# Optimization experiments

Hardware: AMD Instinct MI355X
Metric: run time of the kernel (lower is better)

The kernel has to match this reference:

```python
import jax, jax.numpy as jnp
import numpy as np

V, E_DIM, H_DIR, D_A, C = 50000, 300, 512, 512, 8921  # vocab, embed dim, LSTM hidden per dir, attn dim, classes
B, S = 8, 2048
RNN = 2 * H_DIR  # bidirectional output dim = rnn_dim = 1024


def setup_inputs() -> dict:
    key = jax.random.key(0)
    ks = jax.random.split(key, 13)
    sc = lambda k, shape, s=0.05: (jax.random.normal(k, shape, jnp.float32) * s)
    return {
        "text": jax.random.randint(ks[0], (B, S), 0, V),
        "length": jnp.full((B,), S, dtype=jnp.int32),  # full-length seqs: packing is identity
        "embed": sc(ks[1], (V, E_DIM), 0.1),
        # PyTorch LSTM params, gate order (i, f, g, o); bias folded: b = b_ih + b_hh
        "Wih_f": sc(ks[2], (4 * H_DIR, E_DIM)),
        "Whh_f": sc(ks[3], (4 * H_DIR, H_DIR)),
        "b_f": sc(ks[4], (4 * H_DIR,)),
        "Wih_b": sc(ks[5], (4 * H_DIR, E_DIM)),
        "Whh_b": sc(ks[6], (4 * H_DIR, H_DIR)),
        "b_b": sc(ks[7], (4 * H_DIR,)),
        "Ww": sc(ks[8], (D_A, RNN)),   # self.W: Linear(rnn_dim, d_a, bias=False)
        "Qw": sc(ks[9], (C, D_A)),     # self.Q: Linear(d_a, num_classes, bias=False)
        "Ow": sc(ks[10], (C, RNN)),    # self.output.weight
        "Ob": sc(ks[11], (C,)),        # self.output.bias
    }


def _lstm(x_sbe, Wih, Whh, b, reverse):
    # x_sbe: [S, B, E]; returns hidden states [S, B, H]
    xw = jnp.einsum('sbe,ge->sbg', x_sbe, Wih) + b  # precompute input projections [S,B,4H]
    H = Whh.shape[1]
    Bsz = x_sbe.shape[1]

    def step(carry, g_in):
        h, c = carry
        g = g_in + h @ Whh.T
        i, f, gg, o = jnp.split(g, 4, axis=-1)
        c = jax.nn.sigmoid(f) * c + jax.nn.sigmoid(i) * jnp.tanh(gg)
        h = jax.nn.sigmoid(o) * jnp.tanh(c)
        return (h, c), h

    init = (jnp.zeros((Bsz, H), x_sbe.dtype), jnp.zeros((Bsz, H), x_sbe.dtype))
    _, hs = jax.lax.scan(step, init, xw, reverse=reverse)
    return hs


def reference(text, length, embed, Wih_f, Whh_f, b_f, Wih_b, Whh_b, b_b, Ww, Qw, Ow, Ob):
    # Embedding (eval mode: dropout is identity)
    x = embed[text]                                   # [B,S,E]
    xs = jnp.swapaxes(x, 0, 1)                        # [S,B,E]
    hf = _lstm(xs, Wih_f, Whh_f, b_f, reverse=False)  # [S,B,H]
    hb = _lstm(xs, Wih_b, Whh_b, b_b, reverse=True)   # [S,B,H]
    H = jnp.swapaxes(jnp.concatenate([hf, hb], axis=-1), 0, 1)  # [B,S,rnn_dim]
    # Label-wise attention
    Z = jnp.tanh(jnp.einsum('bsd,ad->bsa', H, Ww))    # [B,S,d_a]
    scores = jnp.einsum('ca,bsa->bcs', Qw, Z)         # [B,C,S]
    alpha = jax.nn.softmax(scores, axis=2)            # softmax over seq
    E = jnp.einsum('bcs,bsd->bcd', alpha, H)          # [B,C,rnn_dim]
    logits = jnp.einsum('cd,bcd->bc', Ow, E) + Ob     # [B,C]
    return logits, alpha
```

## Files before the change

kernel.cpp:

```cpp
#include <hip/hip_runtime.h>
#include <hip/hip_bf16.h>

typedef __attribute__((ext_vector_type(4))) float f32x4;
typedef __attribute__((ext_vector_type(8))) short s16x8;
typedef __attribute__((ext_vector_type(4))) short s16x4;

#define DI __device__ __forceinline__

static constexpr int B_ = 8, S_ = 2048, E_ = 300, EP_ = 320, HD_ = 512, G4_ = 2048;
static constexpr int C_ = 8921, RNN_ = 1024, NROW_ = 16384;

DI float bf2f(unsigned short u){ unsigned int x = ((unsigned int)u) << 16; return __builtin_bit_cast(float, x); }
DI unsigned short f2bf(float f){
  unsigned int x = __builtin_bit_cast(unsigned int, f);
  x += 0x7fff + ((x >> 16) & 1);
  return (unsigned short)(x >> 16);
}
DI float sigm(float x){ return 1.f / (1.f + __expf(-x)); }
DI float tanh_f(float x){
  x = fminf(fmaxf(x, -15.f), 15.f);
  float e = __expf(2.f * x);
  return (e - 1.f) / (e + 1.f);
}
DI void gload16(const void* g, void* l){
  __builtin_amdgcn_global_load_lds((const __attribute__((address_space(1))) void*)g,
                                   (__attribute__((address_space(3))) void*)l, 16, 0, 0);
}
DI unsigned has_sent(unsigned x){
  return (unsigned)(((x & 0xFFFFu) == 0xFFFFu) | ((x >> 16) == 0xFFFFu));
}

__global__ void k_cvt_pad(const float* __restrict__ src, unsigned short* __restrict__ dst,
                          int Rs, int Cs, int Cd){
  int r = blockIdx.x;
  long db = (long)r * Cd;
  for (int c = threadIdx.x; c < Cd; c += blockDim.x){
    float v = (r < Rs && c < Cs) ? src[(long)r * Cs + c] : 0.f;
    dst[db + c] = f2bf(v);
  }
}

__global__ void k_embed(const int* __restrict__ text, const float* __restrict__ emb,
                        unsigned short* __restrict__ xe){
  int m = blockIdx.x;
  int s = m >> 3, b = m & 7;
  int tok = text[b * S_ + s];
  const float* e = emb + (long)tok * E_;
  long db = (long)m * EP_;
  for (int c = threadIdx.x; c < EP_; c += blockDim.x){
    float v = (c < E_) ? e[c] : 0.f;
    xe[db + c] = f2bf(v);
  }
}

template<int EPI>
__global__ __launch_bounds__(256, 2)
void k_gemm_bt(const unsigned short* __restrict__ A, const unsigned short* __restrict__ Bt,
               void* __restrict__ Cout, int N, int K, int Mreal,
               long aBatch, long bBatch, long cBatch, const float* __restrict__ bias){
  __shared__ unsigned short As[128 * 32];
  __shared__ unsigned short Bs[128 * 32];
  const int tid = threadIdx.x, lane = tid & 63, wid = tid >> 6;
  const int wm = wid >> 1, wn = wid & 1;
  const int bm0 = blockIdx.y * 128, bn0 = blockIdx.x * 128;
  A  += (long)blockIdx.z * aBatch;
  Bt += (long)blockIdx.z * bBatch;

  f32x4 acc[4][4];
#pragma unroll
  for (int i = 0; i < 4; ++i)
#pragma unroll
    for (int jx = 0; jx < 4; ++jx) acc[i][jx] = f32x4{0.f, 0.f, 0.f, 0.f};

  for (int k0 = 0; k0 < K; k0 += 32){
    __syncthreads();
#pragma unroll
    for (int cc = 0; cc < 2; ++cc){
      int e = tid + cc * 256;
      int row = e >> 2, seg = e & 3;
      const unsigned short* ga = A + ((long)(bm0 + row)) * K + k0 + seg * 8;
      gload16(ga, (char*)As + cc * 4096 + wid * 1024);
      const unsigned short* gb = Bt + ((long)(bn0 + row)) * K + k0 + seg * 8;
      gload16(gb, (char*)Bs + cc * 4096 + wid * 1024);
    }
    __syncthreads();
    s16x8 af[4], bfr[4];
#pragma unroll
    for (int mt = 0; mt < 4; ++mt){
      int arow = wm * 64 + mt * 16 + (lane & 15);
      af[mt] = *(const s16x8*)((const char*)As + arow * 64 + (lane >> 4) * 16);
    }
#pragma unroll
    for (int nt = 0; nt < 4; ++nt){
      int brow = wn * 64 + nt * 16 + (lane & 15);
      bfr[nt] = *(const s16x8*)((const char*)Bs + brow * 64 + (lane >> 4) * 16);
    }
#pragma unroll
    for (int mt = 0; mt < 4; ++mt)
#pragma unroll
      for (int nt = 0; nt < 4; ++nt)
        acc[mt][nt] = __builtin_amdgcn_mfma_f32_16x16x32_bf16(af[mt], bfr[nt], acc[mt][nt], 0, 0, 0);
  }

  long co = (long)blockIdx.z * cBatch;
#pragma unroll
  for (int mt = 0; mt < 4; ++mt){
#pragma unroll
    for (int r = 0; r < 4; ++r){
      int row = bm0 + wm * 64 + mt * 16 + (lane >> 4) * 4 + r;
      if (row < Mreal){
#pragma unroll
        for (int nt = 0; nt < 4; ++nt){
          int col = bn0 + wn * 64 + nt * 16 + (lane & 15);
          float v = acc[mt][nt][r];
          long idx = co + (long)row * N + col;
          if constexpr (EPI == 0) ((float*)Cout)[idx] = v;
          else if constexpr (EPI == 1) ((unsigned short*)Cout)[idx] = f2bf(tanh_f(v));
          else if constexpr (EPI == 2) ((unsigned short*)Cout)[idx] = f2bf(v + bias[col]);
          else ((unsigned short*)Cout)[idx] = f2bf(v);
        }
      }
    }
  }
}

__global__ __launch_bounds__(256, 1)
void k_lstm(const unsigned short* __restrict__ xw_all,
            const float* __restrict__ Whh_f, const float* __restrict__ Whh_b,
            unsigned short* __restrict__ Hb){
  __shared__ unsigned short hA[16 * 512];
  __shared__ float gl[8 * 128];
  char* hAc = (char*)hA;
  const int tid = threadIdx.x, lane = tid & 63, wave = tid >> 6;
  const int wg = blockIdx.x;
  const int dir = wg >> 4, w16 = wg & 15;
  const int j0 = w16 * 32;
  const int b8 = tid >> 5, j = tid & 31;
  const float* Whh = dir ? Whh_b : Whh_f;
  const unsigned short* xw = xw_all + (long)dir * NROW_ * G4_;

  s16x8 Bf0[16], Bf1[16];
  {
    int lr0 = wave * 32 + (lane & 15);
    int lr1 = lr0 + 16;
    int kg = (lane >> 4) * 8;
    const float* r0 = Whh + (long)((lr0 >> 5) * 512 + j0 + (lr0 & 31)) * 512;
    const float* r1 = Whh + (long)((lr1 >> 5) * 512 + j0 + (lr1 & 31)) * 512;
#pragma unroll
    for (int kt = 0; kt < 16; ++kt){
      s16x8 v0, v1;
#pragma unroll
      for (int i = 0; i < 8; ++i){
        v0[i] = (short)f2bf(r0[kt * 32 + kg + i]);
        v1[i] = (short)f2bf(r1[kt * 32 + kg + i]);
      }
      Bf0[kt] = v0; Bf1[kt] = v1;
    }
  }
  for (int i = tid; i < 16 * 512; i += 256) hA[i] = 0;

  float creg = 0.f;
  float xwi, xwf, xwg, xwo;
  {
    int s0 = dir ? (S_ - 1) : 0;
    long base = ((long)s0 * 8 + b8) * G4_ + j0 + j;
    xwi = bf2f(xw[base]); xwf = bf2f(xw[base + 512]);
    xwg = bf2f(xw[base + 1024]); xwo = bf2f(xw[base + 1536]);
  }
  const int bp0 = tid >> 6, seg0 = tid & 63;
  const int lds0 = (bp0 * 1024 + seg0 * 16) ^ ((bp0 & 7) << 4);
  const int lds1 = ((bp0 + 4) * 1024 + seg0 * 16) ^ (((bp0 + 4) & 7) << 4);
  __syncthreads();

  for (int t = 0; t < S_; ++t){
    int s = dir ? (S_ - 1 - t) : t;
    if (t > 0){
      int sp = dir ? (s + 1) : (s - 1);
      const uint4* gp0 = (const uint4*)(Hb + ((long)bp0 * S_ + sp) * RNN_ + dir * HD_) + seg0;
      const uint4* gp1 = (const uint4*)(Hb + ((long)(bp0 + 4) * S_ + sp) * RNN_ + dir * HD_) + seg0;
      uint4 va0, va1;
      for (;;){
        asm volatile("global_load_dwordx4 %0, %2, off sc0 sc1\n\t"
                     "global_load_dwordx4 %1, %3, off sc0 sc1\n\t"
                     "s_waitcnt vmcnt(0)"
                     : "=&v"(va0), "=&v"(va1) : "v"(gp0), "v"(gp1) : "memory");
        unsigned bad = has_sent(va0.x) | has_sent(va0.y) | has_sent(va0.z) | has_sent(va0.w)
                     | has_sent(va1.x) | has_sent(va1.y) | has_sent(va1.z) | has_sent(va1.w);
        if (!bad) break;
      }
      __builtin_amdgcn_sched_barrier(0);
      *(uint4*)(hAc + lds0) = va0;
      *(uint4*)(hAc + lds1) = va1;
      __syncthreads();
    }

    f32x4 acc0a = {0.f,0.f,0.f,0.f}, acc1a = {0.f,0.f,0.f,0.f};
    f32x4 acc0b = {0.f,0.f,0.f,0.f}, acc1b = {0.f,0.f,0.f,0.f};
    {
      int arow = lane & 15;
      int sw = (arow & 7) << 4;
      int kg16 = (lane >> 4) * 16;
#pragma unroll
      for (int kt = 0; kt < 16; kt += 2){
        int ab0 = (arow * 1024 + kt * 64 + kg16) ^ sw;
        int ab1 = (arow * 1024 + (kt + 1) * 64 + kg16) ^ sw;
        s16x8 afr0 = *(const s16x8*)(hAc + ab0);
        s16x8 afr1 = *(const s16x8*)(hAc + ab1);
        acc0a = __builtin_amdgcn_mfma_f32_16x16x32_bf16(afr0, Bf0[kt], acc0a, 0, 0, 0);
        acc1a = __builtin_amdgcn_mfma_f32_16x16x32_bf16(afr0, Bf1[kt], acc1a, 0, 0, 0);
        acc0b = __builtin_amdgcn_mfma_f32_16x16x32_bf16(afr1, Bf0[kt + 1], acc0b, 0, 0, 0);
        acc1b = __builtin_amdgcn_mfma_f32_16x16x32_bf16(afr1, Bf1[kt + 1], acc1b, 0, 0, 0);
      }
    }
    f32x4 acc0 = acc0a + acc0b, acc1 = acc1a + acc1b;
    {
      int colb = wave * 32 + (lane & 15);
      int rb = (lane >> 4) * 4;
#pragma unroll
      for (int r = 0; r < 4; ++r){
        int row = rb + r;
        if (row < 8){
          gl[row * 128 + colb] = acc0[r];
          gl[row * 128 + colb + 16] = acc1[r];
        }
      }
    }
    __syncthreads();
    {
      float gi = gl[b8 * 128 + j]      + xwi;
      float gf = gl[b8 * 128 + 32 + j] + xwf;
      float gg = gl[b8 * 128 + 64 + j] + xwg;
      float go = gl[b8 * 128 + 96 + j] + xwo;
      creg = sigm(gf) * creg + sigm(gi) * tanh_f(gg);
      float hv = sigm(go) * tanh_f(creg);
      unsigned short* hp = Hb + ((long)b8 * S_ + s) * RNN_ + dir * HD_ + j0 + j;
      unsigned hd = (unsigned)f2bf(hv);
      asm volatile("global_store_short %0, %1, off sc0 sc1"
                   :: "v"(hp), "v"(hd) : "memory");
      if (t + 1 < S_){
        int sn = dir ? (s - 1) : (s + 1);
        long base = ((long)sn * 8 + b8) * G4_ + j0 + j;
        xwi = bf2f(xw[base]); xwf = bf2f(xw[base + 512]);
        xwg = bf2f(xw[base + 1024]); xwo = bf2f(xw[base + 1536]);
      }
    }
  }
}

__global__ __launch_bounds__(256)
void k_softmax_logits(float* __restrict__ alpha, const unsigned short* __restrict__ HOt,
                      const float* __restrict__ Ob, float* __restrict__ logits){
  const int lane = threadIdx.x & 63, wv = threadIdx.x >> 6;
  long row = (long)blockIdx.x * 4 + wv;
  float* a = alpha + row * (long)S_;
  const unsigned short* h = HOt + row * (long)S_;
  float v[32];
  float mx = -1e30f;
#pragma unroll
  for (int jj = 0; jj < 8; ++jj){
    f32x4 t = *(const f32x4*)(a + jj * 256 + lane * 4);
#pragma unroll
    for (int r = 0; r < 4; ++r){ v[jj * 4 + r] = t[r]; mx = fmaxf(mx, t[r]); }
  }
#pragma unroll
  for (int o = 32; o > 0; o >>= 1) mx = fmaxf(mx, __shfl_xor(mx, o));
  float sum = 0.f;
#pragma unroll
  for (int i = 0; i < 32; ++i){ v[i] = __expf(v[i] - mx); sum += v[i]; }
#pragma unroll
  for (int o = 32; o > 0; o >>= 1) sum += __shfl_xor(sum, o);
  float inv = 1.f / sum;
  float dot = 0.f;
#pragma unroll
  for (int jj = 0; jj < 8; ++jj){
    s16x4 hv = *(const s16x4*)(h + jj * 256 + lane * 4);
    f32x4 av;
#pragma unroll
    for (int r = 0; r < 4; ++r){
      float al = v[jj * 4 + r] * inv;
      av[r] = al;
      dot += al * bf2f((unsigned short)hv[r]);
    }
    *(f32x4*)(a + jj * 256 + lane * 4) = av;
  }
#pragma unroll
  for (int o = 32; o > 0; o >>= 1) dot += __shfl_xor(dot, o);
  if (lane == 0){
    int c = (int)(row % C_);
    logits[row] = dot + Ob[c];
  }
}

extern "C" void kernel_launch(void* const* d_in, const int* in_sizes, int n_in,
                              void* d_out, int out_size, void* d_ws, size_t ws_size,
                              hipStream_t stream){
  const int*   text  = (const int*)d_in[0];
  const float* emb   = (const float*)d_in[2];
  const float* Wih_f = (const float*)d_in[3];
  const float* Whh_f = (const float*)d_in[4];
  const float* b_f   = (const float*)d_in[5];
  const float* Wih_b = (const float*)d_in[6];
  const float* Whh_b = (const float*)d_in[7];
  const float* b_b   = (const float*)d_in[8];
  const float* Ww    = (const float*)d_in[9];
  const float* Qw    = (const float*)d_in[10];
  const float* Ow    = (const float*)d_in[11];
  const float* Ob    = (const float*)d_in[12];

  char* ws = (char*)d_ws;
  long o = 0;
  unsigned short* wWihF = (unsigned short*)(ws + o); o += 2048L * 320 * 2;
  unsigned short* wWihB = (unsigned short*)(ws + o); o += 2048L * 320 * 2;
  unsigned short* wWw   = (unsigned short*)(ws + o); o += 512L * 1024 * 2;
  unsigned short* wQw   = (unsigned short*)(ws + o); o += 8960L * 512 * 2;
  unsigned short* wOw   = (unsigned short*)(ws + o); o += 8960L * 1024 * 2;
  unsigned short* wH    = (unsigned short*)(ws + o); o += 8L * 2048 * 1024 * 2;
  unsigned short* wZ    = (unsigned short*)(ws + o); o += 16384L * 512 * 2;
  char* regA = ws + o;
  unsigned short* wXe  = (unsigned short*)regA;
  unsigned short* wXw  = (unsigned short*)(regA + 16384L * 320 * 2);
  unsigned short* wHOt = (unsigned short*)regA;

  float* logits = (float*)d_out;
  float* alpha  = logits + 8L * C_;

  hipMemsetAsync(wH, 0xFF, 8L * 2048 * 1024 * 2, stream);
  k_cvt_pad<<<2048, 256, 0, stream>>>(Wih_f, wWihF, 2048, 300, 320);
  k_cvt_pad<<<2048, 256, 0, stream>>>(Wih_b, wWihB, 2048, 300, 320);
  k_cvt_pad<<<512,  256, 0, stream>>>(Ww, wWw, 512, 1024, 1024);
  k_cvt_pad<<<8960, 256, 0, stream>>>(Qw, wQw, 8921, 512, 512);
  k_cvt_pad<<<8960, 256, 0, stream>>>(Ow, wOw, 8921, 1024, 1024);
  k_embed<<<16384, 256, 0, stream>>>(text, emb, wXe);

  k_gemm_bt<2><<<dim3(16, 128, 1), 256, 0, stream>>>(wXe, wWihF, wXw, 2048, 320, 16384, 0, 0, 0, b_f);
  k_gemm_bt<2><<<dim3(16, 128, 1), 256, 0, stream>>>(wXe, wWihB, wXw + 16384L * 2048, 2048, 320, 16384, 0, 0, 0, b_b);

  k_lstm<<<32, 256, 0, stream>>>(wXw, Whh_f, Whh_b, wH);

  k_gemm_bt<1><<<dim3(4, 128, 1), 256, 0, stream>>>(wH, wWw, wZ, 512, 1024, 16384, 0, 0, 0, nullptr);
  k_gemm_bt<0><<<dim3(16, 70, 8), 256, 0, stream>>>(wQw, wZ, alpha, 2048, 512, C_, 0, 2048L * 512, (long)C_ * 2048, nullptr);
  k_gemm_bt<3><<<dim3(16, 70, 8), 256, 0, stream>>>(wOw, wH, wHOt, 2048, 1024, C_, 0, 2048L * 1024, (long)C_ * 2048, nullptr);

  k_softmax_logits<<<17842, 256, 0, stream>>>(alpha, wHOt, Ob, logits);
}
```

Baseline: 4.887 ms.

## Load LSTM hidden state straight into MFMA registers and drop workgroup barriers

The recurrent LSTM step no longer stages the previous hidden state through shared memory behind a workgroup barrier. Each wave now loads its MFMA A-fragments directly from global memory and owns a private slice of 8 hidden units across all four gates, so the gate exchange runs through a per-wave LDS area with no __syncthreads. The sentinel check is reduced to packed 16-bit max instructions, and pointers are advanced incrementally. The aim is to cut per-timestep barrier and LDS latency on the serial critical path, at the cost of each wave issuing 16 global loads per step, doing redundant reads and spinning on more data.

```diff
diff --git a/kernel.cpp b/kernel.cpp
--- a/kernel.cpp
+++ b/kernel.cpp
@@ -26,9 +26,10 @@
   __builtin_amdgcn_global_load_lds((const __attribute__((address_space(1))) void*)g,
                                    (__attribute__((address_space(3))) void*)l, 16, 0, 0);
 }
-DI unsigned has_sent(unsigned x){
-  return (unsigned)(((x & 0xFFFFu) == 0xFFFFu) | ((x >> 16) == 0xFFFFu));
-}
+DI unsigned pmax16(unsigned a, unsigned b){
+  unsigned r; asm("v_pk_max_u16 %0, %1, %2" : "=v"(r) : "v"(a), "v"(b)); return r;
+}
+DI unsigned pmax4(uint4 v){ return pmax16(pmax16(v.x, v.y), pmax16(v.z, v.w)); }
 
 __global__ void k_cvt_pad(const float* __restrict__ src, unsigned short* __restrict__ dst,
                           int Rs, int Cs, int Cd){
@@ -128,24 +129,24 @@
 void k_lstm(const unsigned short* __restrict__ xw_all,
             const float* __restrict__ Whh_f, const float* __restrict__ Whh_b,
             unsigned short* __restrict__ Hb){
-  __shared__ unsigned short hA[16 * 512];
-  __shared__ float gl[8 * 128];
-  char* hAc = (char*)hA;
+  __shared__ float gl[4 * 8 * 33];
   const int tid = threadIdx.x, lane = tid & 63, wave = tid >> 6;
   const int wg = blockIdx.x;
   const int dir = wg >> 4, w16 = wg & 15;
   const int j0 = w16 * 32;
-  const int b8 = tid >> 5, j = tid & 31;
   const float* Whh = dir ? Whh_b : Whh_f;
   const unsigned short* xw = xw_all + (long)dir * NROW_ * G4_;
 
+  const int b_own = lane >> 3, jj = lane & 7;
+  const int j_own = j0 + wave * 8 + jj;
+
   s16x8 Bf0[16], Bf1[16];
   {
-    int lr0 = wave * 32 + (lane & 15);
-    int lr1 = lr0 + 16;
+    int c = lane & 15;
+    int jd = j0 + wave * 8 + (c & 7);
     int kg = (lane >> 4) * 8;
-    const float* r0 = Whh + (long)((lr0 >> 5) * 512 + j0 + (lr0 & 31)) * 512;
-    const float* r1 = Whh + (long)((lr1 >> 5) * 512 + j0 + (lr1 & 31)) * 512;
+    const float* r0 = Whh + (long)(((c < 8) ? 0 : 512) + jd) * 512;
+    const float* r1 = Whh + (long)(((c < 8) ? 1024 : 1536) + jd) * 512;
 #pragma unroll
     for (int kt = 0; kt < 16; ++kt){
       s16x8 v0, v1;
@@ -157,92 +158,94 @@
       Bf0[kt] = v0; Bf1[kt] = v1;
     }
   }
-  for (int i = tid; i < 16 * 512; i += 256) hA[i] = 0;
+
+  const int s0 = dir ? (S_ - 1) : 0;
+  const long hstep = dir ? -(long)RNN_ : (long)RNN_;
+  const long xstep = dir ? -8L * G4_ : 8L * G4_;
+
+  const unsigned short* xp = xw + ((long)s0 * 8 + b_own) * G4_ + j_own;
+  float xwi = bf2f(xp[0]), xwf = bf2f(xp[512]), xwg = bf2f(xp[1024]), xwo = bf2f(xp[1536]);
+
+  const unsigned short* ab = Hb + ((long)(lane & 7) * S_ + s0) * RNN_ + dir * HD_ + ((lane >> 4) & 3) * 8;
+  unsigned short* hp = Hb + ((long)b_own * S_ + s0) * RNN_ + dir * HD_ + j_own;
+
+  float* glw = gl + wave * (8 * 33);
+  const int c0 = lane & 15;
+  const int bb = (lane >> 4) * 4;
 
   float creg = 0.f;
-  float xwi, xwf, xwg, xwo;
-  {
-    int s0 = dir ? (S_ - 1) : 0;
-    long base = ((long)s0 * 8 + b8) * G4_ + j0 + j;
-    xwi = bf2f(xw[base]); xwf = bf2f(xw[base + 512]);
-    xwg = bf2f(xw[base + 1024]); xwo = bf2f(xw[base + 1536]);
-  }
-  const int bp0 = tid >> 6, seg0 = tid & 63;
-  const int lds0 = (bp0 * 1024 + seg0 * 16) ^ ((bp0 & 7) << 4);
-  const int lds1 = ((bp0 + 4) * 1024 + seg0 * 16) ^ (((bp0 + 4) & 7) << 4);
-  __syncthreads();
 
   for (int t = 0; t < S_; ++t){
-    int s = dir ? (S_ - 1 - t) : t;
-    if (t > 0){
-      int sp = dir ? (s + 1) : (s - 1);
-      const uint4* gp0 = (const uint4*)(Hb + ((long)bp0 * S_ + sp) * RNN_ + dir * HD_) + seg0;
-      const uint4* gp1 = (const uint4*)(Hb + ((long)(bp0 + 4) * S_ + sp) * RNN_ + dir * HD_) + seg0;
-      uint4 va0, va1;
+    float gi, gf, gg, go;
+    if (t == 0){
+      gi = xwi; gf = xwf; gg = xwg; go = xwo;
+    } else {
+      uint4 u[16];
       for (;;){
-        asm volatile("global_load_dwordx4 %0, %2, off sc0 sc1\n\t"
-                     "global_load_dwordx4 %1, %3, off sc0 sc1\n\t"
-                     "s_waitcnt vmcnt(0)"
-                     : "=&v"(va0), "=&v"(va1) : "v"(gp0), "v"(gp1) : "memory");
-        unsigned bad = has_sent(va0.x) | has_sent(va0.y) | has_sent(va0.z) | has_sent(va0.w)
-                     | has_sent(va1.x) | has_sent(va1.y) | has_sent(va1.z) | has_sent(va1.w);
-        if (!bad) break;
-      }
-      __builtin_amdgcn_sched_barrier(0);
-      *(uint4*)(hAc + lds0) = va0;
-      *(uint4*)(hAc + lds1) = va1;
-      __syncthreads();
-    }
-
-    f32x4 acc0a = {0.f,0.f,0.f,0.f}, acc1a = {0.f,0.f,0.f,0.f};
-    f32x4 acc0b = {0.f,0.f,0.f,0.f}, acc1b = {0.f,0.f,0.f,0.f};
-    {
-      int arow = lane & 15;
-      int sw = (arow & 7) << 4;
-      int kg16 = (lane >> 4) * 16;
+        asm volatile(
+          "global_load_dwordx4 %0, %16, off sc0 sc1\n\t"
+          "global_load_dwordx4 %1, %16, off offset:64 sc0 sc1\n\t"
+          "global_load_dwordx4 %2, %16, off offset:128 sc0 sc1\n\t"
+          "global_load_dwordx4 %3, %16, off offset:192 sc0 sc1\n\t"
+          "global_load_dwordx4 %4, %16, off offset:256 sc0 sc1\n\t"
+          "global_load_dwordx4 %5, %16, off offset:320 sc0 sc1\n\t"
+          "global_load_dwordx4 %6, %16, off offset:384 sc0 sc1\n\t"
+          "global_load_dwordx4 %7, %16, off offset:448 sc0 sc1\n\t"
+          "global_load_dwordx4 %8, %16, off offset:512 sc0 sc1\n\t"
+          "global_load_dwordx4 %9, %16, off offset:576 sc0 sc1\n\t"
+          "global_load_dwordx4 %10, %16, off offset:640 sc0 sc1\n\t"
+          "global_load_dwordx4 %11, %16, off offset:704 sc0 sc1\n\t"
+          "global_load_dwordx4 %12, %16, off offset:768 sc0 sc1\n\t"
+          "global_load_dwordx4 %13, %16, off offset:832 sc0 sc1\n\t"
+          "global_load_dwordx4 %14, %16, off offset:896 sc0 sc1\n\t"
+          "global_load_dwordx4 %15, %16, off offset:960 sc0 sc1\n\t"
+          "s_waitcnt vmcnt(0)"
+          : "=&v"(u[0]), "=&v"(u[1]), "=&v"(u[2]), "=&v"(u[3]),
+            "=&v"(u[4]), "=&v"(u[5]), "=&v"(u[6]), "=&v"(u[7]),
+            "=&v"(u[8]), "=&v"(u[9]), "=&v"(u[10]), "=&v"(u[11]),
+            "=&v"(u[12]), "=&v"(u[13]), "=&v"(u[14]), "=&v"(u[15])
+          : "v"(ab) : "memory");
+        unsigned m = pmax16(pmax16(pmax16(pmax4(u[0]), pmax4(u[1])), pmax16(pmax4(u[2]), pmax4(u[3]))),
+                            pmax16(pmax16(pmax4(u[4]), pmax4(u[5])), pmax16(pmax4(u[6]), pmax4(u[7]))));
+        m = pmax16(m, pmax16(pmax16(pmax16(pmax4(u[8]), pmax4(u[9])), pmax16(pmax4(u[10]), pmax4(u[11]))),
+                             pmax16(pmax16(pmax4(u[12]), pmax4(u[13])), pmax16(pmax4(u[14]), pmax4(u[15])))));
+        unsigned mm = (m & 0xFFFFu) > (m >> 16) ? (m & 0xFFFFu) : (m >> 16);
+        if (mm != 0xFFFFu) break;
+      }
+      f32x4 a0a = {0.f,0.f,0.f,0.f}, a0b = a0a, a1a = a0a, a1b = a0a;
 #pragma unroll
       for (int kt = 0; kt < 16; kt += 2){
-        int ab0 = (arow * 1024 + kt * 64 + kg16) ^ sw;
-        int ab1 = (arow * 1024 + (kt + 1) * 64 + kg16) ^ sw;
-        s16x8 afr0 = *(const s16x8*)(hAc + ab0);
-        s16x8 afr1 = *(const s16x8*)(hAc + ab1);
-        acc0a = __builtin_amdgcn_mfma_f32_16x16x32_bf16(afr0, Bf0[kt], acc0a, 0, 0, 0);
-        acc1a = __builtin_amdgcn_mfma_f32_16x16x32_bf16(afr0, Bf1[kt], acc1a, 0, 0, 0);
-        acc0b = __builtin_amdgcn_mfma_f32_16x16x32_bf16(afr1, Bf0[kt + 1], acc0b, 0, 0, 0);
-        acc1b = __builtin_amdgcn_mfma_f32_16x16x32_bf16(afr1, Bf1[kt + 1], acc1b, 0, 0, 0);
-      }
-    }
-    f32x4 acc0 = acc0a + acc0b, acc1 = acc1a + acc1b;
-    {
-      int colb = wave * 32 + (lane & 15);
-      int rb = (lane >> 4) * 4;
-#pragma unroll
-      for (int r = 0; r < 4; ++r){
-        int row = rb + r;
-        if (row < 8){
-          gl[row * 128 + colb] = acc0[r];
-          gl[row * 128 + colb + 16] = acc1[r];
+        s16x8 f0 = __builtin_bit_cast(s16x8, u[kt]);
+        s16x8 f1 = __builtin_bit_cast(s16x8, u[kt + 1]);
+        a0a = __builtin_amdgcn_mfma_f32_16x16x32_bf16(f0, Bf0[kt], a0a, 0, 0, 0);
+        a1a = __builtin_amdgcn_mfma_f32_16x16x32_bf16(f0, Bf1[kt], a1a, 0, 0, 0);
+        a0b = __builtin_amdgcn_mfma_f32_16x16x32_bf16(f1, Bf0[kt + 1], a0b, 0, 0, 0);
+        a1b = __builtin_amdgcn_mfma_f32_16x16x32_bf16(f1, Bf1[kt + 1], a1b, 0, 0, 0);
+      }
+      f32x4 acc0 = a0a + a0b, acc1 = a1a + a1b;
+      if (lane < 32){
+#pragma unroll
+        for (int r = 0; r < 4; ++r){
+          glw[(bb + r) * 33 + c0] = acc0[r];
+          glw[(bb + r) * 33 + 16 + c0] = acc1[r];
         }
       }
-    }
-    __syncthreads();
-    {
-      float gi = gl[b8 * 128 + j]      + xwi;
-      float gf = gl[b8 * 128 + 32 + j] + xwf;
-      float gg = gl[b8 * 128 + 64 + j] + xwg;
-      float go = gl[b8 * 128 + 96 + j] + xwo;
-      creg = sigm(gf) * creg + sigm(gi) * tanh_f(gg);
-      float hv = sigm(go) * tanh_f(creg);
-      unsigned short* hp = Hb + ((long)b8 * S_ + s) * RNN_ + dir * HD_ + j0 + j;
-      unsigned hd = (unsigned)f2bf(hv);
-      asm volatile("global_store_short %0, %1, off sc0 sc1"
-                   :: "v"(hp), "v"(hd) : "memory");
-      if (t + 1 < S_){
-        int sn = dir ? (s - 1) : (s + 1);
-        long base = ((long)sn * 8 + b8) * G4_ + j0 + j;
-        xwi = bf2f(xw[base]); xwf = bf2f(xw[base + 512]);
-        xwg = bf2f(xw[base + 1024]); xwo = bf2f(xw[base + 1536]);
-      }
+      gi = glw[b_own * 33 + jj]      + xwi;
+      gf = glw[b_own * 33 + 8 + jj]  + xwf;
+      gg = glw[b_own * 33 + 16 + jj] + xwg;
+      go = glw[b_own * 33 + 24 + jj] + xwo;
+      ab += hstep;
+    }
+    creg = sigm(gf) * creg + sigm(gi) * tanh_f(gg);
+    float hv = sigm(go) * tanh_f(creg);
+    unsigned hd = (unsigned)f2bf(hv);
+    asm volatile("global_store_short %0, %1, off sc0 sc1"
+                 :: "v"(hp), "v"(hd) : "memory");
+    hp += hstep;
+    if (t + 1 < S_){
+      xp += xstep;
+      xwi = bf2f(xp[0]); xwf = bf2f(xp[512]);
+      xwg = bf2f(xp[1024]); xwo = bf2f(xp[1536]);
     }
   }
 }
```

Result: slower. 9.493 ms (+94.3%).

## Make each wave own its hidden units to drop per-step LSTM block barrier

Applied to the files above, without the earlier changes.

Remaps the Whh rows so each wave computes all four gates for its own 8 hidden units, which lets the gate exchange go through per-wave LDS. This removes the second __syncthreads per time step in the serial recurrence. It also skips the MFMA at t=0, where h is zero. The cost is a different weight-to-lane mapping and reliance on intra-wave LDS ordering, which the code assumes without an explicit wave barrier.

```diff
diff --git a/kernel.cpp b/kernel.cpp
--- a/kernel.cpp
+++ b/kernel.cpp
@@ -129,23 +129,25 @@
             const float* __restrict__ Whh_f, const float* __restrict__ Whh_b,
             unsigned short* __restrict__ Hb){
   __shared__ unsigned short hA[16 * 512];
-  __shared__ float gl[8 * 128];
+  __shared__ float gl[4 * 8 * 33];
   char* hAc = (char*)hA;
   const int tid = threadIdx.x, lane = tid & 63, wave = tid >> 6;
   const int wg = blockIdx.x;
   const int dir = wg >> 4, w16 = wg & 15;
   const int j0 = w16 * 32;
-  const int b8 = tid >> 5, j = tid & 31;
   const float* Whh = dir ? Whh_b : Whh_f;
   const unsigned short* xw = xw_all + (long)dir * NROW_ * G4_;
 
+  const int b_own = lane >> 3, jj = lane & 7;
+  const int j_own = j0 + wave * 8 + jj;
+
   s16x8 Bf0[16], Bf1[16];
   {
-    int lr0 = wave * 32 + (lane & 15);
-    int lr1 = lr0 + 16;
+    int c = lane & 15;
+    int jd = j0 + wave * 8 + (c & 7);
     int kg = (lane >> 4) * 8;
-    const float* r0 = Whh + (long)((lr0 >> 5) * 512 + j0 + (lr0 & 31)) * 512;
-    const float* r1 = Whh + (long)((lr1 >> 5) * 512 + j0 + (lr1 & 31)) * 512;
+    const float* r0 = Whh + (long)(((c < 8) ? 0 : 512) + jd) * 512;
+    const float* r1 = Whh + (long)(((c < 8) ? 1024 : 1536) + jd) * 512;
 #pragma unroll
     for (int kt = 0; kt < 16; ++kt){
       s16x8 v0, v1;
@@ -159,22 +161,30 @@
   }
   for (int i = tid; i < 16 * 512; i += 256) hA[i] = 0;
 
+  const int s0 = dir ? (S_ - 1) : 0;
+
   float creg = 0.f;
   float xwi, xwf, xwg, xwo;
   {
-    int s0 = dir ? (S_ - 1) : 0;
-    long base = ((long)s0 * 8 + b8) * G4_ + j0 + j;
+    long base = ((long)s0 * 8 + b_own) * G4_ + j_own;
     xwi = bf2f(xw[base]); xwf = bf2f(xw[base + 512]);
     xwg = bf2f(xw[base + 1024]); xwo = bf2f(xw[base + 1536]);
   }
   const int bp0 = tid >> 6, seg0 = tid & 63;
   const int lds0 = (bp0 * 1024 + seg0 * 16) ^ ((bp0 & 7) << 4);
   const int lds1 = ((bp0 + 4) * 1024 + seg0 * 16) ^ (((bp0 + 4) & 7) << 4);
+
+  float* glw = gl + wave * (8 * 33);
+  const int c0 = lane & 15;
+  const int bb = (lane >> 4) * 4;
   __syncthreads();
 
   for (int t = 0; t < S_; ++t){
     int s = dir ? (S_ - 1 - t) : t;
-    if (t > 0){
+    float gi, gf, gg, go;
+    if (t == 0){
+      gi = xwi; gf = xwf; gg = xwg; go = xwo;
+    } else {
       int sp = dir ? (s + 1) : (s - 1);
       const uint4* gp0 = (const uint4*)(Hb + ((long)bp0 * S_ + sp) * RNN_ + dir * HD_) + seg0;
       const uint4* gp1 = (const uint4*)(Hb + ((long)(bp0 + 4) * S_ + sp) * RNN_ + dir * HD_) + seg0;
@@ -192,57 +202,48 @@
       *(uint4*)(hAc + lds0) = va0;
       *(uint4*)(hAc + lds1) = va1;
       __syncthreads();
-    }
-
-    f32x4 acc0a = {0.f,0.f,0.f,0.f}, acc1a = {0.f,0.f,0.f,0.f};
-    f32x4 acc0b = {0.f,0.f,0.f,0.f}, acc1b = {0.f,0.f,0.f,0.f};
-    {
-      int arow = lane & 15;
-      int sw = (arow & 7) << 4;
-      int kg16 = (lane >> 4) * 16;
-#pragma unroll
-      for (int kt = 0; kt < 16; kt += 2){
-        int ab0 = (arow * 1024 + kt * 64 + kg16) ^ sw;
-        int ab1 = (arow * 1024 + (kt + 1) * 64 + kg16) ^ sw;
-        s16x8 afr0 = *(const s16x8*)(hAc + ab0);
-        s16x8 afr1 = *(const s16x8*)(hAc + ab1);
-        acc0a = __builtin_amdgcn_mfma_f32_16x16x32_bf16(afr0, Bf0[kt], acc0a, 0, 0, 0);
-        acc1a = __builtin_amdgcn_mfma_f32_16x16x32_bf16(afr0, Bf1[kt], acc1a, 0, 0, 0);
-        acc0b = __builtin_amdgcn_mfma_f32_16x16x32_bf16(afr1, Bf0[kt + 1], acc0b, 0, 0, 0);
-        acc1b = __builtin_amdgcn_mfma_f32_16x16x32_bf16(afr1, Bf1[kt + 1], acc1b, 0, 0, 0);
-      }
-    }
-    f32x4 acc0 = acc0a + acc0b, acc1 = acc1a + acc1b;
-    {
-      int colb = wave * 32 + (lane & 15);
-      int rb = (lane >> 4) * 4;
-#pragma unroll
-      for (int r = 0; r < 4; ++r){
-        int row = rb + r;
-        if (row < 8){
-          gl[row * 128 + colb] = acc0[r];
-          gl[row * 128 + colb + 16] = acc1[r];
+
+      f32x4 a0a = {0.f,0.f,0.f,0.f}, a0b = a0a, a1a = a0a, a1b = a0a;
+      {
+        int arow = lane & 15;
+        int sw = (arow & 7) << 4;
+        int kg16 = (lane >> 4) * 16;
+#pragma unroll
+        for (int kt = 0; kt < 16; kt += 2){
+          int ab0 = (arow * 1024 + kt * 64 + kg16) ^ sw;
+          int ab1 = (arow * 1024 + (kt + 1) * 64 + kg16) ^ sw;
+          s16x8 afr0 = *(const s16x8*)(hAc + ab0);
+          s16x8 afr1 = *(const s16x8*)(hAc + ab1);
+          a0a = __builtin_amdgcn_mfma_f32_16x16x32_bf16(afr0, Bf0[kt], a0a, 0, 0, 0);
+          a1a = __builtin_amdgcn_mfma_f32_16x16x32_bf16(afr0, Bf1[kt], a1a, 0, 0, 0);
+          a0b = __builtin_amdgcn_mfma_f32_16x16x32_bf16(afr1, Bf0[kt + 1], a0b, 0, 0, 0);
+          a1b = __builtin_amdgcn_mfma_f32_16x16x32_bf16(afr1, Bf1[kt + 1], a1b, 0, 0, 0);
         }
       }
-    }
-    __syncthreads();
-    {
-      float gi = gl[b8 * 128 + j]      + xwi;
-      float gf = gl[b8 * 128 + 32 + j] + xwf;
-      float gg = gl[b8 * 128 + 64 + j] + xwg;
-      float go = gl[b8 * 128 + 96 + j] + xwo;
-      creg = sigm(gf) * creg + sigm(gi) * tanh_f(gg);
-      float hv = sigm(go) * tanh_f(creg);
-      unsigned short* hp = Hb + ((long)b8 * S_ + s) * RNN_ + dir * HD_ + j0 + j;
-      unsigned hd = (unsigned)f2bf(hv);
-      asm volatile("global_store_short %0, %1, off sc0 sc1"
-                   :: "v"(hp), "v"(hd) : "memory");
-      if (t + 1 < S_){
-        int sn = dir ? (s - 1) : (s + 1);
-        long base = ((long)sn * 8 + b8) * G4_ + j0 + j;
-        xwi = bf2f(xw[base]); xwf = bf2f(xw[base + 512]);
-        xwg = bf2f(xw[base + 1024]); xwo = bf2f(xw[base + 1536]);
-      }
+      f32x4 acc0 = a0a + a0b, acc1 = a1a + a1b;
+      if (lane < 32){
+#pragma unroll
+        for (int r = 0; r < 4; ++r){
+          glw[(bb + r) * 33 + c0] = acc0[r];
+          glw[(bb + r) * 33 + 16 + c0] = acc1[r];
+        }
+      }
+      gi = glw[b_own * 33 + jj]      + xwi;
+      gf = glw[b_own * 33 + 8 + jj]  + xwf;
+      gg = glw[b_own * 33 + 16 + jj] + xwg;
+      go = glw[b_own * 33 + 24 + jj] + xwo;
+    }
+    creg = sigm(gf) * creg + sigm(gi) * tanh_f(gg);
+    float hv = sigm(go) * tanh_f(creg);
+    unsigned short* hp = Hb + ((long)b_own * S_ + s) * RNN_ + dir * HD_ + j_own;
+    unsigned hd = (unsigned)f2bf(hv);
+    asm volatile("global_store_short %0, %1, off sc0 sc1"
+                 :: "v"(hp), "v"(hd) : "memory");
+    if (t + 1 < S_){
+      int sn = dir ? (s - 1) : (s + 1);
+      long base = ((long)sn * 8 + b_own) * G4_ + j_own;
+      xwi = bf2f(xw[base]); xwf = bf2f(xw[base + 512]);
+      xwg = bf2f(xw[base + 1024]); xwo = bf2f(xw[base + 1536]);
     }
   }
 }
```

Result: slower. 4.998 ms (+2.3%).

## Pin LSTM direction workgroups to single XCDs via atomic role claiming

Applied to the files above, without the earlier changes.

The LSTM kernel now launches 256 workgroups, and each reads its XCC ID. Workgroups on XCC 0 claim forward-direction roles and those on XCC 1 claim backward roles through atomic counters, and the surplus ones exit. The aim is to keep each direction's 16 cooperating workgroups on one XCD so the cross-workgroup hidden-state polling stays within a shared L2. The spin loop also skips the system-coherent sc1 bit on most iterations. This depends on the hardware scheduling enough blocks onto each XCD, with a sleeping fallback, and it is a deadlock risk if the claimants are not co-resident.

```diff
diff --git a/kernel.cpp b/kernel.cpp
--- a/kernel.cpp
+++ b/kernel.cpp
@@ -127,13 +127,32 @@
 __global__ __launch_bounds__(256, 1)
 void k_lstm(const unsigned short* __restrict__ xw_all,
             const float* __restrict__ Whh_f, const float* __restrict__ Whh_b,
-            unsigned short* __restrict__ Hb){
+            unsigned short* __restrict__ Hb, int* __restrict__ claim){
   __shared__ unsigned short hA[16 * 512];
   __shared__ float gl[8 * 128];
+  __shared__ int roleSh;
   char* hAc = (char*)hA;
   const int tid = threadIdx.x, lane = tid & 63, wave = tid >> 6;
-  const int wg = blockIdx.x;
-  const int dir = wg >> 4, w16 = wg & 15;
+
+  unsigned xcc;
+  asm volatile("s_getreg_b32 %0, hwreg(HW_REG_XCC_ID)" : "=s"(xcc));
+  xcc &= 7;
+  if (tid == 0){
+    int r = -1;
+    if (xcc == 0){ int c = atomicAdd(&claim[0], 1); if (c < 16) r = c; }
+    else if (xcc == 1){ int c = atomicAdd(&claim[1], 1); if (c < 16) r = 16 + c; }
+    if (r < 0){
+      for (int i = 0; i < 30; ++i) __builtin_amdgcn_s_sleep(127);
+      int c = atomicAdd(&claim[0], 1); if (c < 16) r = c;
+      if (r < 0){ c = atomicAdd(&claim[1], 1); if (c < 16) r = 16 + c; }
+    }
+    roleSh = r;
+  }
+  __syncthreads();
+  const int role = roleSh;
+  if (role < 0) return;
+
+  const int dir = role >> 4, w16 = role & 15;
   const int j0 = w16 * 32;
   const int b8 = tid >> 5, j = tid & 31;
   const float* Whh = dir ? Whh_b : Whh_f;
@@ -179,11 +198,18 @@
       const uint4* gp0 = (const uint4*)(Hb + ((long)bp0 * S_ + sp) * RNN_ + dir * HD_) + seg0;
       const uint4* gp1 = (const uint4*)(Hb + ((long)(bp0 + 4) * S_ + sp) * RNN_ + dir * HD_) + seg0;
       uint4 va0, va1;
-      for (;;){
-        asm volatile("global_load_dwordx4 %0, %2, off sc0 sc1\n\t"
-                     "global_load_dwordx4 %1, %3, off sc0 sc1\n\t"
-                     "s_waitcnt vmcnt(0)"
-                     : "=&v"(va0), "=&v"(va1) : "v"(gp0), "v"(gp1) : "memory");
+      for (int it = 0;; ++it){
+        if ((it & 7) == 7){
+          asm volatile("global_load_dwordx4 %0, %2, off sc0 sc1\n\t"
+                       "global_load_dwordx4 %1, %3, off sc0 sc1\n\t"
+                       "s_waitcnt vmcnt(0)"
+                       : "=&v"(va0), "=&v"(va1) : "v"(gp0), "v"(gp1) : "memory");
+        } else {
+          asm volatile("global_load_dwordx4 %0, %2, off sc0\n\t"
+                       "global_load_dwordx4 %1, %3, off sc0\n\t"
+                       "s_waitcnt vmcnt(0)"
+                       : "=&v"(va0), "=&v"(va1) : "v"(gp0), "v"(gp1) : "memory");
+        }
         unsigned bad = has_sent(va0.x) | has_sent(va0.y) | has_sent(va0.z) | has_sent(va0.w)
                      | has_sent(va1.x) | has_sent(va1.y) | has_sent(va1.z) | has_sent(va1.w);
         if (!bad) break;
@@ -316,6 +342,7 @@
   unsigned short* wOw   = (unsigned short*)(ws + o); o += 8960L * 1024 * 2;
   unsigned short* wH    = (unsigned short*)(ws + o); o += 8L * 2048 * 1024 * 2;
   unsigned short* wZ    = (unsigned short*)(ws + o); o += 16384L * 512 * 2;
+  int* wClaim           = (int*)(ws + o);            o += 64;
   char* regA = ws + o;
   unsigned short* wXe  = (unsigned short*)regA;
   unsigned short* wXw  = (unsigned short*)(regA + 16384L * 320 * 2);
@@ -325,6 +352,7 @@
   float* alpha  = logits + 8L * C_;
 
   hipMemsetAsync(wH, 0xFF, 8L * 2048 * 1024 * 2, stream);
+  hipMemsetAsync(wClaim, 0, 64, stream);
   k_cvt_pad<<<2048, 256, 0, stream>>>(Wih_f, wWihF, 2048, 300, 320);
   k_cvt_pad<<<2048, 256, 0, stream>>>(Wih_b, wWihB, 2048, 300, 320);
   k_cvt_pad<<<512,  256, 0, stream>>>(Ww, wWw, 512, 1024, 1024);
@@ -335,7 +363,7 @@
   k_gemm_bt<2><<<dim3(16, 128, 1), 256, 0, stream>>>(wXe, wWihF, wXw, 2048, 320, 16384, 0, 0, 0, b_f);
   k_gemm_bt<2><<<dim3(16, 128, 1), 256, 0, stream>>>(wXe, wWihB, wXw + 16384L * 2048, 2048, 320, 16384, 0, 0, 0, b_b);
 
-  k_lstm<<<32, 256, 0, stream>>>(wXw, Whh_f, Whh_b, wH);
+  k_lstm<<<256, 256, 0, stream>>>(wXw, Whh_f, Whh_b, wH, wClaim);
 
   k_gemm_bt<1><<<dim3(4, 128, 1), 256, 0, stream>>>(wH, wWw, wZ, 512, 1024, 16384, 0, 0, 0, nullptr);
   k_gemm_bt<0><<<dim3(16, 70, 8), 256, 0, stream>>>(wQw, wZ, alpha, 2048, 512, C_, 0, 2048L * 512, (long)C_ * 2048, nullptr);
```

New measurement: 6.303 ms. 1.29x slower.
